# Kernel optimization log

Hardware: AMD Instinct MI355X
Metric: run time of the kernel (lower is better)

Reference implementation:

```python
import jax, jax.numpy as jnp
import numpy as np

B, N, C, H = 4, 2048, 1024, 16
DH = C // H
SCALE = DH ** -0.5


def setup_inputs() -> dict:
    key = jax.random.key(0)
    ks = jax.random.split(key, 5)
    s = C ** -0.5
    return {
        "x": jax.random.normal(ks[0], (B, N, C), dtype=jnp.float32),
        "Wq": jax.random.normal(ks[1], (C, C), dtype=jnp.float32) * s,
        "Wkv": jax.random.normal(ks[2], (C, 2 * C), dtype=jnp.float32) * s,
        "Wout": jax.random.normal(ks[3], (C, C), dtype=jnp.float32) * s,
        "bout": jax.random.normal(ks[4], (C,), dtype=jnp.float32) * 0.01,
    }


def reference(x, Wq, Wkv, Wout, bout):
    b, n, c = x.shape
    # projections (torch Linear: x @ W.T, here we store W already as [in,out])
    q = (x @ Wq).reshape(b, n, H, DH).transpose(0, 2, 1, 3)  # b h n d
    kv = x @ Wkv
    k, v = jnp.split(kv, 2, axis=-1)
    k = k.reshape(b, n, H, DH).transpose(0, 2, 1, 3)
    v = v.reshape(b, n, H, DH).transpose(0, 2, 1, 3)
    sim = jnp.einsum("bhnd,bhmd->bhnm", q, k) * SCALE
    attn = jax.nn.softmax(sim, axis=-1)
    out = jnp.einsum("bhnm,bhmd->bhnd", attn, v)
    out = out.transpose(0, 2, 1, 3).reshape(b, n, c)
    return out @ Wout + bout
```

## Files before the change

### kernel.cpp

```cpp
#include <hip/hip_runtime.h>
#include <stdint.h>

typedef unsigned short u16;
typedef unsigned int u32;
typedef __attribute__((ext_vector_type(8))) short bf16x8;
typedef __attribute__((ext_vector_type(8))) unsigned short u16x8;
typedef __attribute__((ext_vector_type(4))) float f32x4;

#define B_DIM 4
#define N_DIM 2048
#define C_DIM 1024
#define H_DIM 16
#define M_DIM (B_DIM * N_DIM)
#define ATT_SCALE 0.125f

__device__ __forceinline__ u16 f2bf(float f) {
  u32 u = __builtin_bit_cast(u32, f);
  return (u16)((u + 0x7FFFu + ((u >> 16) & 1u)) >> 16);
}

__device__ __forceinline__ void gload16(const void* g, void* l) {
  __builtin_amdgcn_global_load_lds(
      (const __attribute__((address_space(1))) u32*)g,
      (__attribute__((address_space(3))) u32*)l, 16, 0, 0);
}

__global__ void cast_bf16_kernel(const float* __restrict__ in, u16* __restrict__ out, int n4) {
  int i = blockIdx.x * blockDim.x + threadIdx.x;
  int stride = gridDim.x * blockDim.x;
  for (; i < n4; i += stride) {
    float4 v = ((const float4*)in)[i];
    ushort4 o;
    o.x = f2bf(v.x); o.y = f2bf(v.y); o.z = f2bf(v.z); o.w = f2bf(v.w);
    ((ushort4*)out)[i] = o;
  }
}

__global__ void tcast_kernel(const float* __restrict__ W, u16* __restrict__ Wt, int K, int N) {
  __shared__ float tile[32][33];
  int n0 = blockIdx.x * 32, k0 = blockIdx.y * 32;
  int tx = threadIdx.x, ty = threadIdx.y;
  #pragma unroll
  for (int i = 0; i < 32; i += 8)
    tile[ty + i][tx] = W[(size_t)(k0 + ty + i) * N + (n0 + tx)];
  __syncthreads();
  #pragma unroll
  for (int i = 0; i < 32; i += 8)
    Wt[(size_t)(n0 + ty + i) * K + (k0 + tx)] = f2bf(tile[tx][ty + i]);
}

template <int MODE>
__global__ __launch_bounds__(256) void gemm_bt_kernel(
    const u16* __restrict__ A, const u16* __restrict__ Bt, void* __restrict__ Cout,
    const float* __restrict__ bias, u16* __restrict__ vt, int K, int N) {
  __shared__ __align__(16) char lds[16384];
  const int tid  = threadIdx.x;
  const int lane = tid & 63, w = tid >> 6;
  const int lr = lane & 15, g = lane >> 4;
  const int m0 = blockIdx.y * 128, n0 = blockIdx.x * 128;
  const int wm = w >> 1, wn = w & 1;

  f32x4 acc[4][4] = {};
  const int nkt = K >> 5;
  const int rsub = lane >> 2;
  const int csub = lane & 3;
  for (int kt = 0; kt < nkt; ++kt) {
    #pragma unroll
    for (int j = 0; j < 2; ++j) {
      int rowblk = w * 2 + j;
      int row = rowblk * 16 + rsub;
      gload16(A  + (size_t)(m0 + row) * K + kt * 32 + csub * 8, lds + rowblk * 1024);
      gload16(Bt + (size_t)(n0 + row) * K + kt * 32 + csub * 8, lds + 8192 + rowblk * 1024);
    }
    __syncthreads();
    bf16x8 a[4], b[4];
    #pragma unroll
    for (int m = 0; m < 4; ++m)
      a[m] = *(const bf16x8*)(lds + ((wm * 64 + m * 16 + lr) * 64 + g * 16));
    #pragma unroll
    for (int n = 0; n < 4; ++n)
      b[n] = *(const bf16x8*)(lds + 8192 + ((wn * 64 + n * 16 + lr) * 64 + g * 16));
    #pragma unroll
    for (int m = 0; m < 4; ++m)
      #pragma unroll
      for (int n = 0; n < 4; ++n)
        acc[m][n] = __builtin_amdgcn_mfma_f32_16x16x32_bf16(a[m], b[n], acc[m][n], 0, 0, 0);
    __syncthreads();
  }
  #pragma unroll
  for (int m = 0; m < 4; ++m) {
    #pragma unroll
    for (int n = 0; n < 4; ++n) {
      int col  = n0 + wn * 64 + n * 16 + lr;
      int row0 = m0 + wm * 64 + m * 16 + g * 4;
      if constexpr (MODE == 1) {
        #pragma unroll
        for (int r = 0; r < 4; ++r)
          ((float*)Cout)[(size_t)(row0 + r) * N + col] = acc[m][n][r] + bias[col];
      } else if constexpr (MODE == 0) {
        #pragma unroll
        for (int r = 0; r < 4; ++r)
          ((u16*)Cout)[(size_t)(row0 + r) * N + col] = f2bf(acc[m][n][r]);
      } else {
        if (col < 1024) {
          #pragma unroll
          for (int r = 0; r < 4; ++r)
            ((u16*)Cout)[(size_t)(row0 + r) * 1024 + col] = f2bf(acc[m][n][r]);
        } else {
          int cc = col - 1024;
          int hh = cc >> 6, d = cc & 63;
          int bb = row0 >> 11, nn = row0 & 2047;
          ushort4 pkv;
          pkv.x = f2bf(acc[m][n][0]); pkv.y = f2bf(acc[m][n][1]);
          pkv.z = f2bf(acc[m][n][2]); pkv.w = f2bf(acc[m][n][3]);
          *(ushort4*)(vt + ((size_t)(bb * 16 + hh) * 64 + d) * 2048 + nn) = pkv;
        }
      }
    }
  }
}

__global__ __launch_bounds__(256) void attn_kernel(
    const u16* __restrict__ Qb, const u16* __restrict__ Kb,
    const u16* __restrict__ Vt, u16* __restrict__ AO) {
  __shared__ __align__(16) char lds[51200];
  const int tid  = threadIdx.x;
  const int lane = tid & 63, w = tid >> 6;
  const int lr = lane & 15, g = lane >> 4;
  const int lin = blockIdx.x;
  const int nid = (lin & 7) * 128 + (lin >> 3);
  const int bh = nid >> 4;
  const int b = bh >> 4, h = bh & 15;
  const int q0 = (nid & 15) * 128 + w * 32;
  const size_t rowbase = (size_t)b * N_DIM;

  bf16x8 qf[2][2];
  #pragma unroll
  for (int qs = 0; qs < 2; ++qs)
    #pragma unroll
    for (int kb = 0; kb < 2; ++kb)
      qf[qs][kb] = *(const bf16x8*)(Qb + (rowbase + q0 + qs * 16 + lr) * C_DIM + h * 64 + kb * 32 + g * 8);

  f32x4 accO[2][4] = {};
  float lsum[2] = {0.f, 0.f};

  char* Pl = lds + 32768 + w * 4608;

  auto STAGE = [&](int kt, int buf) {
    #pragma unroll
    for (int j = 0; j < 2; ++j) {
      int c = (w * 2 + j) * 64 + lane;
      int row = c >> 3, slot = (c & 7) ^ (row & 7);
      gload16(Kb + (size_t)(rowbase + kt * 64 + row) * 1024 + h * 64 + slot * 8,
              lds + buf * 8192 + (w * 2 + j) * 1024);
      gload16(Vt + ((size_t)bh * 64 + row) * 2048 + kt * 64 + slot * 8,
              lds + 16384 + buf * 8192 + (w * 2 + j) * 1024);
    }
  };

  STAGE(0, 0);
  __syncthreads();

  for (int kt = 0; kt < N_DIM / 64; ++kt) {
    if (kt + 1 < N_DIM / 64) STAGE(kt + 1, (kt + 1) & 1);
    const char* K_ = lds + (kt & 1) * 8192;
    const char* V_ = lds + 16384 + (kt & 1) * 8192;

    bf16x8 kfr[4][2];
    #pragma unroll
    for (int kf = 0; kf < 4; ++kf)
      #pragma unroll
      for (int kb = 0; kb < 2; ++kb)
        kfr[kf][kb] = *(const bf16x8*)(K_ + (kf * 16 + lr) * 128 + (((kb * 4 + g) ^ (lr & 7)) << 4));
    f32x4 st[2][4] = {};
    #pragma unroll
    for (int qs = 0; qs < 2; ++qs)
      #pragma unroll
      for (int kf = 0; kf < 4; ++kf)
        #pragma unroll
        for (int kb = 0; kb < 2; ++kb)
          st[qs][kf] = __builtin_amdgcn_mfma_f32_16x16x32_bf16(kfr[kf][kb], qf[qs][kb], st[qs][kf], 0, 0, 0);

    #pragma unroll
    for (int qs = 0; qs < 2; ++qs) {
      #pragma unroll
      for (int kf = 0; kf < 4; ++kf) {
        float e0 = __expf(st[qs][kf][0] * ATT_SCALE);
        float e1 = __expf(st[qs][kf][1] * ATT_SCALE);
        float e2 = __expf(st[qs][kf][2] * ATT_SCALE);
        float e3 = __expf(st[qs][kf][3] * ATT_SCALE);
        lsum[qs] += (e0 + e1) + (e2 + e3);
        u32 r0, r1;
        asm("v_cvt_pk_bf16_f32 %0, %1, %2" : "=v"(r0) : "v"(e0), "v"(e1));
        asm("v_cvt_pk_bf16_f32 %0, %1, %2" : "=v"(r1) : "v"(e2), "v"(e3));
        uint2 pk; pk.x = r0; pk.y = r1;
        *(uint2*)(Pl + (qs * 16 + lr) * 144 + kf * 32 + g * 8) = pk;
      }
    }

    bf16x8 vfr[4][2];
    #pragma unroll
    for (int nf = 0; nf < 4; ++nf)
      #pragma unroll
      for (int kb = 0; kb < 2; ++kb)
        vfr[nf][kb] = *(const bf16x8*)(V_ + (nf * 16 + lr) * 128 + (((kb * 4 + g) ^ (lr & 7)) << 4));
    #pragma unroll
    for (int qs = 0; qs < 2; ++qs) {
      #pragma unroll
      for (int kb = 0; kb < 2; ++kb) {
        bf16x8 pa = *(const bf16x8*)(Pl + (qs * 16 + lr) * 144 + kb * 64 + g * 16);
        #pragma unroll
        for (int nf = 0; nf < 4; ++nf)
          accO[qs][nf] = __builtin_amdgcn_mfma_f32_16x16x32_bf16(pa, vfr[nf][kb], accO[qs][nf], 0, 0, 0);
      }
    }
    __syncthreads();
  }

  #pragma unroll
  for (int qs = 0; qs < 2; ++qs) {
    lsum[qs] += __shfl_xor(lsum[qs], 16);
    lsum[qs] += __shfl_xor(lsum[qs], 32);
    #pragma unroll
    for (int r = 0; r < 4; ++r) {
      float ls = __shfl(lsum[qs], (4 * g + r) | (g << 4));
      float inv = 1.0f / ls;
      int q = q0 + qs * 16 + 4 * g + r;
      #pragma unroll
      for (int nf = 0; nf < 4; ++nf)
        AO[(rowbase + q) * C_DIM + h * 64 + nf * 16 + lr] = f2bf(accO[qs][nf][r] * inv);
    }
  }
}

extern "C" void kernel_launch(void* const* d_in, const int* in_sizes, int n_in,
                              void* d_out, int out_size, void* d_ws, size_t ws_size,
                              hipStream_t stream) {
  (void)in_sizes; (void)n_in; (void)out_size; (void)ws_size;
  const float* x    = (const float*)d_in[0];
  const float* Wq   = (const float*)d_in[1];
  const float* Wkv  = (const float*)d_in[2];
  const float* Wout = (const float*)d_in[3];
  const float* bout = (const float*)d_in[4];
  float* out = (float*)d_out;

  char* ws = (char*)d_ws;
  u16* xb   = (u16*)(ws);
  u16* wqT  = (u16*)(ws + (16u << 20));
  u16* wkvT = (u16*)(ws + (18u << 20));
  u16* woT  = (u16*)(ws + (22u << 20));
  u16* q    = (u16*)(ws + (24u << 20));
  u16* kbuf = (u16*)(ws + (40u << 20));
  u16* vT   = (u16*)(ws + (56u << 20));
  u16* ao   = xb;

  cast_bf16_kernel<<<2048, 256, 0, stream>>>(x, xb, M_DIM * C_DIM / 4);
  dim3 tb(32, 8);
  tcast_kernel<<<dim3(C_DIM / 32,     C_DIM / 32), tb, 0, stream>>>(Wq,   wqT,  C_DIM, C_DIM);
  tcast_kernel<<<dim3(2 * C_DIM / 32, C_DIM / 32), tb, 0, stream>>>(Wkv,  wkvT, C_DIM, 2 * C_DIM);
  tcast_kernel<<<dim3(C_DIM / 32,     C_DIM / 32), tb, 0, stream>>>(Wout, woT,  C_DIM, C_DIM);

  gemm_bt_kernel<0><<<dim3(C_DIM / 128,     M_DIM / 128), 256, 0, stream>>>(xb, wqT,  q,    nullptr, nullptr, C_DIM, C_DIM);
  gemm_bt_kernel<2><<<dim3(2 * C_DIM / 128, M_DIM / 128), 256, 0, stream>>>(xb, wkvT, kbuf, nullptr, vT,      C_DIM, 2 * C_DIM);

  attn_kernel<<<dim3(N_DIM / 128 * B_DIM * H_DIM), 256, 0, stream>>>(q, kbuf, vT, ao);

  gemm_bt_kernel<1><<<dim3(C_DIM / 128, M_DIM / 128), 256, 0, stream>>>(ao, woT, out, bout, nullptr, C_DIM, C_DIM);
}
```

Baseline: 244.1 us.

## Fuse Q and KV projections; fold softmax scale into Q; MFMA row sums

The Q and KV projection GEMMs become a single launch over N=3072. This relies on the transposed Wq and Wkv buffers sitting back to back in the workspace, so their rows form one contiguous B matrix. The Q output is pre-multiplied by scale*log2(e), which lets the attention kernel use a raw exp2 with no per-element multiply. The softmax denominator is now accumulated with an extra MFMA against a ones vector instead of VALU adds and cross-lane shuffles, and the final normalization uses a fast reciprocal. The trade is fewer launches and less VALU work against extra matrix-core instructions, plus row sums taken from the bf16-rounded probabilities.

After: 222.5 us. 8.8% less time.

```diff
diff --git a/kernel.cpp b/kernel.cpp
--- a/kernel.cpp
+++ b/kernel.cpp
@@ -12,7 +12,7 @@
 #define C_DIM 1024
 #define H_DIM 16
 #define M_DIM (B_DIM * N_DIM)
-#define ATT_SCALE 0.125f
+#define QSCALE 0.18033688011112042f
 
 __device__ __forceinline__ u16 f2bf(float f) {
   u32 u = __builtin_bit_cast(u32, f);
@@ -52,7 +52,8 @@
 template <int MODE>
 __global__ __launch_bounds__(256) void gemm_bt_kernel(
     const u16* __restrict__ A, const u16* __restrict__ Bt, void* __restrict__ Cout,
-    const float* __restrict__ bias, u16* __restrict__ vt, int K, int N) {
+    const float* __restrict__ bias, u16* __restrict__ vt, u16* __restrict__ aux,
+    int K, int N) {
   __shared__ __align__(16) char lds[16384];
   const int tid  = threadIdx.x;
   const int lane = tid & 63, w = tid >> 6;
@@ -97,17 +98,18 @@
         #pragma unroll
         for (int r = 0; r < 4; ++r)
           ((float*)Cout)[(size_t)(row0 + r) * N + col] = acc[m][n][r] + bias[col];
-      } else if constexpr (MODE == 0) {
-        #pragma unroll
-        for (int r = 0; r < 4; ++r)
-          ((u16*)Cout)[(size_t)(row0 + r) * N + col] = f2bf(acc[m][n][r]);
       } else {
         if (col < 1024) {
           #pragma unroll
           for (int r = 0; r < 4; ++r)
-            ((u16*)Cout)[(size_t)(row0 + r) * 1024 + col] = f2bf(acc[m][n][r]);
+            ((u16*)Cout)[(size_t)(row0 + r) * 1024 + col] = f2bf(acc[m][n][r] * QSCALE);
+        } else if (col < 2048) {
+          int cc = col - 1024;
+          #pragma unroll
+          for (int r = 0; r < 4; ++r)
+            aux[(size_t)(row0 + r) * 1024 + cc] = f2bf(acc[m][n][r]);
         } else {
-          int cc = col - 1024;
+          int cc = col - 2048;
           int hh = cc >> 6, d = cc & 63;
           int bb = row0 >> 11, nn = row0 & 2047;
           ushort4 pkv;
@@ -141,9 +143,12 @@
     for (int kb = 0; kb < 2; ++kb)
       qf[qs][kb] = *(const bf16x8*)(Qb + (rowbase + q0 + qs * 16 + lr) * C_DIM + h * 64 + kb * 32 + g * 8);
 
+  bf16x8 onesb;
+  #pragma unroll
+  for (int j = 0; j < 8; ++j) onesb[j] = (short)0x3F80;
+
   f32x4 accO[2][4] = {};
-  float lsum[2] = {0.f, 0.f};
-
+  f32x4 accSum[2] = {};
   char* Pl = lds + 32768 + w * 4608;
 
   auto STAGE = [&](int kt, int buf) {
@@ -185,11 +190,10 @@
     for (int qs = 0; qs < 2; ++qs) {
       #pragma unroll
       for (int kf = 0; kf < 4; ++kf) {
-        float e0 = __expf(st[qs][kf][0] * ATT_SCALE);
-        float e1 = __expf(st[qs][kf][1] * ATT_SCALE);
-        float e2 = __expf(st[qs][kf][2] * ATT_SCALE);
-        float e3 = __expf(st[qs][kf][3] * ATT_SCALE);
-        lsum[qs] += (e0 + e1) + (e2 + e3);
+        float e0 = __builtin_amdgcn_exp2f(st[qs][kf][0]);
+        float e1 = __builtin_amdgcn_exp2f(st[qs][kf][1]);
+        float e2 = __builtin_amdgcn_exp2f(st[qs][kf][2]);
+        float e3 = __builtin_amdgcn_exp2f(st[qs][kf][3]);
         u32 r0, r1;
         asm("v_cvt_pk_bf16_f32 %0, %1, %2" : "=v"(r0) : "v"(e0), "v"(e1));
         asm("v_cvt_pk_bf16_f32 %0, %1, %2" : "=v"(r1) : "v"(e2), "v"(e3));
@@ -209,6 +213,7 @@
       #pragma unroll
       for (int kb = 0; kb < 2; ++kb) {
         bf16x8 pa = *(const bf16x8*)(Pl + (qs * 16 + lr) * 144 + kb * 64 + g * 16);
+        accSum[qs] = __builtin_amdgcn_mfma_f32_16x16x32_bf16(pa, onesb, accSum[qs], 0, 0, 0);
         #pragma unroll
         for (int nf = 0; nf < 4; ++nf)
           accO[qs][nf] = __builtin_amdgcn_mfma_f32_16x16x32_bf16(pa, vfr[nf][kb], accO[qs][nf], 0, 0, 0);
@@ -218,19 +223,15 @@
   }
 
   #pragma unroll
-  for (int qs = 0; qs < 2; ++qs) {
-    lsum[qs] += __shfl_xor(lsum[qs], 16);
-    lsum[qs] += __shfl_xor(lsum[qs], 32);
+  for (int qs = 0; qs < 2; ++qs)
     #pragma unroll
     for (int r = 0; r < 4; ++r) {
-      float ls = __shfl(lsum[qs], (4 * g + r) | (g << 4));
-      float inv = 1.0f / ls;
+      float inv = __builtin_amdgcn_rcpf(accSum[qs][r]);
       int q = q0 + qs * 16 + 4 * g + r;
       #pragma unroll
       for (int nf = 0; nf < 4; ++nf)
         AO[(rowbase + q) * C_DIM + h * 64 + nf * 16 + lr] = f2bf(accO[qs][nf][r] * inv);
     }
-  }
 }
 
 extern "C" void kernel_launch(void* const* d_in, const int* in_sizes, int n_in,
@@ -260,10 +261,11 @@
   tcast_kernel<<<dim3(2 * C_DIM / 32, C_DIM / 32), tb, 0, stream>>>(Wkv,  wkvT, C_DIM, 2 * C_DIM);
   tcast_kernel<<<dim3(C_DIM / 32,     C_DIM / 32), tb, 0, stream>>>(Wout, woT,  C_DIM, C_DIM);
 
-  gemm_bt_kernel<0><<<dim3(C_DIM / 128,     M_DIM / 128), 256, 0, stream>>>(xb, wqT,  q,    nullptr, nullptr, C_DIM, C_DIM);
-  gemm_bt_kernel<2><<<dim3(2 * C_DIM / 128, M_DIM / 128), 256, 0, stream>>>(xb, wkvT, kbuf, nullptr, vT,      C_DIM, 2 * C_DIM);
+  gemm_bt_kernel<3><<<dim3(3 * C_DIM / 128, M_DIM / 128), 256, 0, stream>>>(
+      xb, wqT, q, nullptr, vT, kbuf, C_DIM, 3 * C_DIM);
 
   attn_kernel<<<dim3(N_DIM / 128 * B_DIM * H_DIM), 256, 0, stream>>>(q, kbuf, vT, ao);
 
-  gemm_bt_kernel<1><<<dim3(C_DIM / 128, M_DIM / 128), 256, 0, stream>>>(ao, woT, out, bout, nullptr, C_DIM, C_DIM);
-}
+  gemm_bt_kernel<1><<<dim3(C_DIM / 128, M_DIM / 128), 256, 0, stream>>>(
+      ao, woT, out, bout, nullptr, nullptr, C_DIM, C_DIM);
+}
```
